# Optimization experiments

Hardware: AMD Instinct MI355X
Metric: run time of the kernel (lower is better)

The kernel has to match this reference:

```python
import jax, jax.numpy as jnp
import numpy as np

B = 8192          # batch (parallel RL envs)
LATENT = 32       # latent_size
CIN = 128         # original input_size (obs dim), c features
HID = 256         # hidden_size
ACT = 16          # num_actions
E = 8             # num_experts
GH = 128          # gate hidden size (hardcoded in module)
IN0 = LATENT + CIN    # layer-0 input dim (160)
INTER = HID + LATENT  # layer-1/2 input dim (288)
LN_EPS = 1e-5


def setup_inputs() -> dict:
    key = jax.random.key(0)
    ks = jax.random.split(key, 10)
    s = lambda k, shape, scale=1.0: jax.random.normal(k, shape, jnp.float32) * scale
    return {
        "z": s(ks[0], (B, LATENT)),
        "c": s(ks[1], (B, CIN)),
        # expert MLP params (kaiming-like small uniform scale stand-in)
        "w0": s(ks[2], (E, IN0, HID), 0.05),   "b0": jnp.full((E, HID), 0.01, jnp.float32),
        "w1": s(ks[3], (E, INTER, HID), 0.05), "b1": jnp.full((E, HID), 0.01, jnp.float32),
        "w2": s(ks[4], (E, INTER, ACT), 0.05), "b2": jnp.full((E, ACT), 0.01, jnp.float32),
        # gate MLP params
        "g0w": s(ks[5], (IN0, GH), 0.05), "g0b": jnp.zeros((GH,), jnp.float32),
        "g1w": s(ks[6], (GH, GH), 0.05),  "g1b": jnp.zeros((GH,), jnp.float32),
        "g2w": s(ks[7], (GH, E), 0.05),   "g2b": jnp.zeros((E,), jnp.float32),
        # LayerNorm on c
        "ln_g": jnp.ones((CIN,), jnp.float32),
        "ln_b": jnp.zeros((CIN,), jnp.float32),
    }


def _layer_norm(x, g, b):
    m = x.mean(-1, keepdims=True)
    v = ((x - m) ** 2).mean(-1, keepdims=True)
    return (x - m) / jnp.sqrt(v + LN_EPS) * g + b


def reference(z, c, w0, b0, w1, b1, w2, b2, g0w, g0b, g1w, g1b, g2w, g2b, ln_g, ln_b):
    cn = _layer_norm(c, ln_g, ln_b)                      # [B, CIN]
    x = jnp.concatenate([z, cn], axis=1)                 # [B, IN0]
    # gate: Linear-ELU-Linear-ELU-Linear, softmax over experts
    h = jax.nn.elu(x @ g0w + g0b)
    h = jax.nn.elu(h @ g1w + g1b)
    coeff = jax.nn.softmax(h @ g2w + g2b, axis=1)        # [B, E]

    layer_out = cn
    for w, b, act in ((w0, b0, True), (w1, b1, True), (w2, b2, False)):
        inp = jnp.concatenate([z, layer_out], axis=1)    # [B, in_dim]
        # per-expert GEMM then soft-mix (same math as coeff-mixed weight @ input)
        per = jnp.einsum('bi,eio->beo', inp, w)          # [B, E, out_dim]
        out = jnp.einsum('be,beo->bo', coeff, per) + coeff @ b  # [B, out_dim]
        layer_out = jax.nn.elu(out) if act else out
    return layer_out
```

## Files before the change

kernel.cpp:

```cpp
#include <hip/hip_runtime.h>
#include <math.h>

#define B_     8192
#define LATENT 32
#define CIN    128
#define HID    256
#define ACTD   16
#define NE     8
#define GH     128
#define IN0    160
#define INTER  288

typedef __attribute__((ext_vector_type(8))) _Float16 half8;
typedef __attribute__((ext_vector_type(4))) float    f32x4;
typedef __attribute__((ext_vector_type(4))) int      i32x4;

__device__ __forceinline__ float elu1(float x) { return x > 0.0f ? x : expm1f(x); }

__device__ __forceinline__ void gload16(const void* g, const char* lds) {
    __builtin_amdgcn_global_load_lds((const __attribute__((address_space(1))) void*)g,
                                     (__attribute__((address_space(3))) void*)lds, 16, 0, 0);
}
__device__ __forceinline__ half8 as_h8(i32x4 v) {
    union U { i32x4 a; half8 b; } u; u.a = v; return u.b;
}

__global__ __launch_bounds__(256) void k_prep_ln(
    const float* __restrict__ w0, const float* __restrict__ w1, const float* __restrict__ w2,
    const float* __restrict__ g0w, const float* __restrict__ g1w,
    const float* __restrict__ z, const float* __restrict__ c,
    const float* __restrict__ g, const float* __restrict__ bt,
    _Float16* __restrict__ T0, _Float16* __restrict__ T1, _Float16* __restrict__ T2,
    _Float16* __restrict__ G0, _Float16* __restrict__ G1,
    _Float16* __restrict__ X0, _Float16* __restrict__ X1, _Float16* __restrict__ X2)
{
    if (blockIdx.x < 484) {
        int gq = blockIdx.x * 256 + threadIdx.x;
        const float* src; int stride; size_t dst; _Float16* H;
        if (gq < 40960) {
            int e = gq / 5120, r = gq % 5120, o = r / 20, i0 = (r % 20) * 8;
            src = w0 + ((size_t)e * 160 + i0) * 256 + o; stride = 256;
            dst = ((size_t)e * 256 + o) * 160 + i0; H = T0;
        } else if (gq < 114688) {
            int t = gq - 40960;
            int e = t / 9216, r = t % 9216, o = r / 36, i0 = (r % 36) * 8;
            src = w1 + ((size_t)e * 288 + i0) * 256 + o; stride = 256;
            dst = ((size_t)e * 256 + o) * 288 + i0; H = T1;
        } else if (gq < 119296) {
            int t = gq - 114688;
            int e = t / 576, r = t % 576, o = r / 36, i0 = (r % 36) * 8;
            src = w2 + ((size_t)e * 288 + i0) * 16 + o; stride = 16;
            dst = ((size_t)e * 16 + o) * 288 + i0; H = T2;
        } else if (gq < 121856) {
            int t = gq - 119296;
            int o = t / 20, i0 = (t % 20) * 8;
            src = g0w + (size_t)i0 * 128 + o; stride = 128;
            dst = (size_t)o * 160 + i0; H = G0;
        } else if (gq < 123904) {
            int t = gq - 121856;
            int o = t / 16, i0 = (t % 16) * 8;
            src = g1w + (size_t)i0 * 128 + o; stride = 128;
            dst = (size_t)o * 128 + i0; H = G1;
        } else return;
        _Float16 hh[8];
        #pragma unroll
        for (int j = 0; j < 8; ++j) hh[j] = (_Float16)src[(size_t)j * stride];
        *(half8*)&H[dst] = *(const half8*)hh;
        return;
    }
    int gid = (blockIdx.x - 484) * 256 + threadIdx.x;
    int row = gid >> 6;
    int l = threadIdx.x & 63;
    const float* cr = c + (size_t)row * CIN;
    float v0 = cr[l], v1 = cr[l + 64];
    float s = v0 + v1;
    #pragma unroll
    for (int o = 32; o; o >>= 1) s += __shfl_xor(s, o);
    float mean = s * (1.0f / 128.0f);
    float d0 = v0 - mean, d1 = v1 - mean;
    float q = d0 * d0 + d1 * d1;
    #pragma unroll
    for (int o = 32; o; o >>= 1) q += __shfl_xor(q, o);
    float rstd = rsqrtf(q * (1.0f / 128.0f) + 1e-5f);
    float y0 = d0 * rstd * g[l] + bt[l];
    float y1 = d1 * rstd * g[l + 64] + bt[l + 64];
    size_t r0 = (size_t)row * IN0;
    X0[r0 + 32 + l] = (_Float16)y0;
    X0[r0 + 96 + l] = (_Float16)y1;
    if (l < LATENT) {
        _Float16 zv = (_Float16)z[(size_t)row * LATENT + l];
        X0[r0 + l] = zv;
        size_t r1 = (size_t)row * INTER;
        X1[r1 + l] = zv;
        X2[r1 + l] = zv;
    }
}

__global__ __launch_bounds__(128, 2) void k_gate_fused(
    const _Float16* __restrict__ X0, const _Float16* __restrict__ G0T,
    const _Float16* __restrict__ G1T,
    const float* __restrict__ g0b, const float* __restrict__ g1b,
    const float* __restrict__ g2w, const float* __restrict__ g2b,
    float* __restrict__ coeff)
{
    __shared__ __align__(16) char smem[86016];
    const int tid = threadIdx.x, wid = tid >> 6, l = tid & 63;
    const int brow = blockIdx.x * 32;
    const int rl16 = wid * 16;

    char* sG1  = smem + 40960;
    char* h1   = smem + 73728;
    float* wt_t = (float*)(smem + 81920);

    const int swz = (((l & 3) ^ ((l >> 3) & 3)) << 3);
    const int rq  = l >> 2;
    const int rdo = ((l & 15) << 6) + (((l >> 4) ^ ((l >> 1) & 3)) << 4);

    #pragma unroll
    for (int p = 0; p < 40; ++p) {
        if ((p & 1) != wid) continue;
        const int ks = p / 8, gg = p % 8;
        gload16(G0T + (size_t)(gg * 16 + rq) * IN0 + ks * 32 + swz, smem + p * 1024);
    }
    #pragma unroll
    for (int p = 0; p < 32; ++p) {
        if ((p & 1) != wid) continue;
        const int ks = p / 8, gg = p % 8;
        gload16(G1T + (size_t)(gg * 16 + rq) * GH + ks * 32 + swz, sG1 + p * 1024);
    }
    const _Float16* Ar0 = X0 + (size_t)(brow + rl16 + (l & 15)) * IN0 + (l >> 4) * 8;
    i32x4 a0[5];
    #pragma unroll
    for (int ks = 0; ks < 5; ++ks) a0[ks] = *(const i32x4*)(Ar0 + ks * 32);
    for (int idx = tid; idx < 1024; idx += 128)
        wt_t[(idx & 7) * 128 + (idx >> 3)] = g2w[(idx >> 3) * 8 + (idx & 7)];
    __syncthreads();

    f32x4 acc[8];
    #pragma unroll
    for (int nf = 0; nf < 8; ++nf) {
        float bv = g0b[nf * 16 + (l & 15)];
        acc[nf] = (f32x4){bv, bv, bv, bv};
    }
    #pragma unroll
    for (int ks = 0; ks < 5; ++ks)
        #pragma unroll
        for (int nf = 0; nf < 8; ++nf) {
            half8 b = *(const half8*)(smem + (size_t)(ks * 8 + nf) * 1024 + rdo);
            acc[nf] = __builtin_amdgcn_mfma_f32_16x16x32_f16(as_h8(a0[ks]), b, acc[nf], 0, 0, 0);
        }

    #pragma unroll
    for (int nf = 0; nf < 8; ++nf)
        #pragma unroll
        for (int r = 0; r < 4; ++r) {
            const int rloc = ((l >> 4) << 2) + r;
            const int row = rl16 + rloc;
            const int colb = (nf * 16 + (l & 15)) * 2;
            *(_Float16*)(h1 + row * 256 + (colb ^ ((rloc & 7) << 4))) = (_Float16)elu1(acc[nf][r]);
        }
    __syncthreads();

    i32x4 a1[4];
    #pragma unroll
    for (int ks = 0; ks < 4; ++ks) {
        const int row = rl16 + (l & 15);
        const int off = (ks * 64 + ((l >> 4) << 4)) ^ ((row & 7) << 4);
        a1[ks] = *(const i32x4*)(h1 + row * 256 + off);
    }

    #pragma unroll
    for (int nf = 0; nf < 8; ++nf) {
        float bv = g1b[nf * 16 + (l & 15)];
        acc[nf] = (f32x4){bv, bv, bv, bv};
    }
    #pragma unroll
    for (int ks = 0; ks < 4; ++ks)
        #pragma unroll
        for (int nf = 0; nf < 8; ++nf) {
            half8 b = *(const half8*)(sG1 + (size_t)(ks * 8 + nf) * 1024 + rdo);
            acc[nf] = __builtin_amdgcn_mfma_f32_16x16x32_f16(as_h8(a1[ks]), b, acc[nf], 0, 0, 0);
        }

    float pe[8][4];
    #pragma unroll
    for (int e = 0; e < 8; ++e)
        #pragma unroll
        for (int r = 0; r < 4; ++r) pe[e][r] = 0.f;
    #pragma unroll
    for (int nf = 0; nf < 8; ++nf) {
        float w_[8];
        #pragma unroll
        for (int e = 0; e < 8; ++e) w_[e] = wt_t[e * 128 + nf * 16 + (l & 15)];
        #pragma unroll
        for (int r = 0; r < 4; ++r) {
            float hv = elu1(acc[nf][r]);
            #pragma unroll
            for (int e = 0; e < 8; ++e) pe[e][r] = fmaf(hv, w_[e], pe[e][r]);
        }
    }
    #pragma unroll
    for (int off = 1; off < 16; off <<= 1)
        #pragma unroll
        for (int e = 0; e < 8; ++e)
            #pragma unroll
            for (int r = 0; r < 4; ++r) pe[e][r] += __shfl_xor(pe[e][r], off);

    if ((l & 15) == 0) {
        #pragma unroll
        for (int r = 0; r < 4; ++r) {
            float pv[8];
            float mx = -1e30f;
            #pragma unroll
            for (int e = 0; e < 8; ++e) { pv[e] = pe[e][r] + g2b[e]; mx = fmaxf(mx, pv[e]); }
            float s = 0.f;
            #pragma unroll
            for (int e = 0; e < 8; ++e) { pv[e] = expf(pv[e] - mx); s += pv[e]; }
            float inv = 1.0f / s;
            const int row = brow + rl16 + ((l >> 4) << 2) + r;
            #pragma unroll
            for (int e = 0; e < 8; ++e) coeff[(size_t)row * 8 + e] = pv[e] * inv;
        }
    }
}

template<int KS>
__global__ __launch_bounds__(256, 3) void k_moe_epar(
    const _Float16* __restrict__ A, const _Float16* __restrict__ Bw,
    const float* __restrict__ bias,
    const float* __restrict__ coeff,
    _Float16* __restrict__ outX)
{
    constexpr int K = KS * 32;
    __shared__ __align__(16) char smem[43008];

    const int tid = threadIdx.x, wid = tid >> 6, l = tid & 63;
    const int brow = (blockIdx.x & 127) * 64;
    const int bn   = (blockIdx.x >> 7) * 32;

    float* cfl = (float*)(smem + 40960);
    if (tid < 128) {
        f32x4 v = *(const f32x4*)&coeff[(size_t)(brow + (tid >> 1)) * 8 + (tid & 1) * 4];
        *(f32x4*)&cfl[tid * 4] = v;
    }

    const int swz = (((l & 3) ^ ((l >> 3) & 3)) << 3);
    const int rq  = l >> 2;
    const _Float16* sA = A + (size_t)(brow + wid * 16 + rq) * K + swz;
    const _Float16* sB2[2][2];
    #pragma unroll
    for (int e2 = 0; e2 < 2; ++e2)
        #pragma unroll
        for (int gg = 0; gg < 2; ++gg)
            sB2[e2][gg] = Bw + (size_t)((2 * wid + e2) * HID + bn + gg * 16 + rq) * K + swz;

    auto stage = [&](int bi, int k0) {
        char* buf = smem + bi * 20480;
        gload16(sA + k0, buf + wid * 1024);
        #pragma unroll
        for (int e2 = 0; e2 < 2; ++e2)
            #pragma unroll
            for (int gg = 0; gg < 2; ++gg)
                gload16(sB2[e2][gg] + k0,
                        buf + 4096 + (2 * wid + e2) * 2048 + gg * 1024);
    };

    const int rdo = ((l & 15) << 6) + (((l >> 4) ^ ((l >> 1) & 3)) << 4);
    f32x4 acc[2][4][2];
    #pragma unroll
    for (int e2 = 0; e2 < 2; ++e2)
        #pragma unroll
        for (int mf = 0; mf < 4; ++mf)
            #pragma unroll
            for (int nf = 0; nf < 2; ++nf) acc[e2][mf][nf] = (f32x4){0.f, 0.f, 0.f, 0.f};

    stage(0, 0);
    if (KS > 1) stage(1, 32);
    __syncthreads();

    for (int t = 0; t < KS; ++t) {
        const char* buf = smem + (t & 1) * 20480;
        half8 af[4], b0[2], b1[2];
        #pragma unroll
        for (int mf = 0; mf < 4; ++mf)
            af[mf] = *(const half8*)(buf + mf * 1024 + rdo);
        #pragma unroll
        for (int e2 = 0; e2 < 2; ++e2) {
            const char* be = buf + 4096 + (2 * wid + e2) * 2048;
            b0[e2] = *(const half8*)(be + rdo);
            b1[e2] = *(const half8*)(be + 1024 + rdo);
        }
        asm volatile("s_waitcnt lgkmcnt(0)" ::: "memory");
        __builtin_amdgcn_sched_barrier(0);
        __builtin_amdgcn_s_barrier();
        if (t + 2 < KS) stage(t & 1, (t + 2) * 32);
        __builtin_amdgcn_sched_barrier(0);

        __builtin_amdgcn_s_setprio(1);
        #pragma unroll
        for (int e2 = 0; e2 < 2; ++e2)
            #pragma unroll
            for (int mf = 0; mf < 4; ++mf) {
                acc[e2][mf][0] = __builtin_amdgcn_mfma_f32_16x16x32_f16(af[mf], b0[e2], acc[e2][mf][0], 0, 0, 0);
                acc[e2][mf][1] = __builtin_amdgcn_mfma_f32_16x16x32_f16(af[mf], b1[e2], acc[e2][mf][1], 0, 0, 0);
            }
        __builtin_amdgcn_s_setprio(0);

        if (t + 1 < KS) {
            if (t + 2 < KS) { asm volatile("s_waitcnt vmcnt(5)" ::: "memory"); }
            else            { asm volatile("s_waitcnt vmcnt(0)" ::: "memory"); }
            __builtin_amdgcn_s_barrier();
            __builtin_amdgcn_sched_barrier(0);
        }
    }

    const int e0 = 2 * wid, e1 = 2 * wid + 1;
    float bv0[2], bv1[2];
    #pragma unroll
    for (int nf = 0; nf < 2; ++nf) {
        bv0[nf] = bias[e0 * HID + bn + nf * 16 + (l & 15)];
        bv1[nf] = bias[e1 * HID + bn + nf * 16 + (l & 15)];
    }
    __syncthreads();
    float* red = (float*)smem;
    #pragma unroll
    for (int mf = 0; mf < 4; ++mf) {
        const int rb = mf * 16 + ((l >> 4) << 2);
        #pragma unroll
        for (int r = 0; r < 4; ++r) {
            float c0 = cfl[(rb + r) * 8 + e0];
            float c1 = cfl[(rb + r) * 8 + e1];
            #pragma unroll
            for (int nf = 0; nf < 2; ++nf) {
                float s = (acc[0][mf][nf][r] + bv0[nf]) * c0
                        + (acc[1][mf][nf][r] + bv1[nf]) * c1;
                red[wid * 2304 + (rb + r) * 36 + nf * 16 + (l & 15)] = s;
            }
        }
    }
    __syncthreads();

    const int row = tid >> 2, c0_ = (tid & 3) * 8;
    f32x4 s0 = {0.f, 0.f, 0.f, 0.f}, s1 = {0.f, 0.f, 0.f, 0.f};
    #pragma unroll
    for (int w = 0; w < 4; ++w) {
        s0 += *(const f32x4*)&red[w * 2304 + row * 36 + c0_];
        s1 += *(const f32x4*)&red[w * 2304 + row * 36 + c0_ + 4];
    }
    _Float16 hh[8];
    #pragma unroll
    for (int j = 0; j < 4; ++j) {
        hh[j]     = (_Float16)elu1(s0[j]);
        hh[4 + j] = (_Float16)elu1(s1[j]);
    }
    size_t o = (size_t)(brow + row) * INTER + 32 + bn + c0_;
    *(half8*)&outX[o] = *(const half8*)hh;
}

__global__ __launch_bounds__(128, 2) void k_final(
    const _Float16* __restrict__ X2, const _Float16* __restrict__ T2,
    const float* __restrict__ b2, const float* __restrict__ cf,
    float* __restrict__ out)
{
    __shared__ __align__(16) char smem[73728];
    const int tid = threadIdx.x, wid = tid >> 6, l = tid & 63;
    const int brow = blockIdx.x * 32;

    const _Float16* Ar = X2 + (size_t)(brow + wid * 16 + (l & 15)) * INTER + (l >> 4) * 8;
    i32x4 a_[9];
    #pragma unroll
    for (int ks = 0; ks < 9; ++ks) a_[ks] = *(const i32x4*)(Ar + ks * 32);

    const int swz = (((l & 3) ^ ((l >> 3) & 3)) << 3);
    const int rq  = l >> 2;
    #pragma unroll
    for (int p = 0; p < 72; ++p) {
        if ((p & 1) != wid) continue;
        const int ks = p / 8, gg = p % 8;
        gload16(T2 + (size_t)(gg * 16 + rq) * INTER + ks * 32 + swz, smem + p * 1024);
    }

    const int rdo = ((l & 15) << 6) + (((l >> 4) ^ ((l >> 1) & 3)) << 4);
    f32x4 acc[8];
    #pragma unroll
    for (int nf = 0; nf < 8; ++nf) {
        float bv = b2[nf * 16 + (l & 15)];
        acc[nf] = (f32x4){bv, bv, bv, bv};
    }
    #pragma unroll
    for (int ks = 0; ks < 9; ++ks) {
        switch (ks) {
            case 0: asm volatile("s_waitcnt vmcnt(32)" ::: "memory"); break;
            case 1: asm volatile("s_waitcnt vmcnt(28)" ::: "memory"); break;
            case 2: asm volatile("s_waitcnt vmcnt(24)" ::: "memory"); break;
            case 3: asm volatile("s_waitcnt vmcnt(20)" ::: "memory"); break;
            case 4: asm volatile("s_waitcnt vmcnt(16)" ::: "memory"); break;
            case 5: asm volatile("s_waitcnt vmcnt(12)" ::: "memory"); break;
            case 6: asm volatile("s_waitcnt vmcnt(8)"  ::: "memory"); break;
            case 7: asm volatile("s_waitcnt vmcnt(4)"  ::: "memory"); break;
            default: asm volatile("s_waitcnt vmcnt(0)" ::: "memory"); break;
        }
        __builtin_amdgcn_s_barrier();
        __builtin_amdgcn_sched_barrier(0);
        if (ks == 0) {
            #pragma unroll
            for (int k2 = 0; k2 < 9; ++k2) asm volatile("" : "+v"(a_[k2]));
        }
        #pragma unroll
        for (int nf = 0; nf < 8; ++nf) {
            half8 b = *(const half8*)(smem + (size_t)(ks * 8 + nf) * 1024 + rdo);
            acc[nf] = __builtin_amdgcn_mfma_f32_16x16x32_f16(as_h8(a_[ks]), b, acc[nf], 0, 0, 0);
        }
    }

    #pragma unroll
    for (int r = 0; r < 4; ++r) {
        const int row = brow + wid * 16 + ((l >> 4) << 2) + r;
        const float* cr = cf + (size_t)row * 8;
        float s = 0.f;
        #pragma unroll
        for (int e = 0; e < 8; ++e) s = fmaf(cr[e], acc[e][r], s);
        out[(size_t)row * ACTD + (l & 15)] = s;
    }
}

extern "C" void kernel_launch(void* const* d_in, const int* in_sizes, int n_in,
                              void* d_out, int out_size, void* d_ws, size_t ws_size,
                              hipStream_t stream)
{
    (void)in_sizes; (void)n_in; (void)out_size; (void)ws_size;
    const float* z   = (const float*)d_in[0];
    const float* c   = (const float*)d_in[1];
    const float* w0  = (const float*)d_in[2];
    const float* b0  = (const float*)d_in[3];
    const float* w1  = (const float*)d_in[4];
    const float* b1  = (const float*)d_in[5];
    const float* w2  = (const float*)d_in[6];
    const float* b2  = (const float*)d_in[7];
    const float* g0w = (const float*)d_in[8];
    const float* g0b = (const float*)d_in[9];
    const float* g1w = (const float*)d_in[10];
    const float* g1b = (const float*)d_in[11];
    const float* g2w = (const float*)d_in[12];
    const float* g2b = (const float*)d_in[13];
    const float* lng = (const float*)d_in[14];
    const float* lnb = (const float*)d_in[15];
    float* out = (float*)d_out;

    char* p = (char*)d_ws;
    auto alloc = [&](size_t n) { char* r = p; p += (n + 255) & ~(size_t)255; return r; };
    _Float16* X0  = (_Float16*)alloc((size_t)B_ * IN0 * 2);
    _Float16* X1  = (_Float16*)alloc((size_t)B_ * INTER * 2);
    _Float16* X2  = (_Float16*)alloc((size_t)B_ * INTER * 2);
    float* cf  = (float*)alloc((size_t)B_ * NE * 4);
    _Float16* T0  = (_Float16*)alloc((size_t)NE * IN0 * HID * 2);
    _Float16* T1  = (_Float16*)alloc((size_t)NE * INTER * HID * 2);
    _Float16* T2  = (_Float16*)alloc((size_t)NE * INTER * ACTD * 2);
    _Float16* G0T = (_Float16*)alloc((size_t)IN0 * GH * 2);
    _Float16* G1T = (_Float16*)alloc((size_t)GH * GH * 2);

    k_prep_ln<<<dim3(484 + B_ / 4), dim3(256), 0, stream>>>(
        w0, w1, w2, g0w, g1w, z, c, lng, lnb,
        T0, T1, T2, G0T, G1T, X0, X1, X2);

    k_gate_fused<<<dim3(256), dim3(128), 0, stream>>>(
        X0, G0T, G1T, g0b, g1b, g2w, g2b, cf);

    k_moe_epar<5><<<dim3(1024), dim3(256), 0, stream>>>(X0, T0, b0, cf, X1);
    k_moe_epar<9><<<dim3(1024), dim3(256), 0, stream>>>(X1, T1, b1, cf, X2);

    k_final<<<dim3(256), dim3(128), 0, stream>>>(X2, T2, b2, cf, out);
}
```

Baseline: 65.29 us.

## Replace double-buffered BK32 MoE pipeline with single-buffer BK64 stages

After: 68.58 us. 5.1% more time.

```diff
diff --git a/kernel.cpp b/kernel.cpp
--- a/kernel.cpp
+++ b/kernel.cpp
@@ -225,13 +225,14 @@
 }
 
 template<int KS>
-__global__ __launch_bounds__(256, 3) void k_moe_epar(
+__global__ __launch_bounds__(256, 3) void k_moe_bk64(
     const _Float16* __restrict__ A, const _Float16* __restrict__ Bw,
     const float* __restrict__ bias,
     const float* __restrict__ coeff,
     _Float16* __restrict__ outX)
 {
-    constexpr int K = KS * 32;
+    constexpr int K  = KS * 32;
+    constexpr int NP = (KS + 1) / 2;
     __shared__ __align__(16) char smem[43008];
 
     const int tid = threadIdx.x, wid = tid >> 6, l = tid & 63;
@@ -254,15 +255,19 @@
         for (int gg = 0; gg < 2; ++gg)
             sB2[e2][gg] = Bw + (size_t)((2 * wid + e2) * HID + bn + gg * 16 + rq) * K + swz;
 
-    auto stage = [&](int bi, int k0) {
-        char* buf = smem + bi * 20480;
-        gload16(sA + k0, buf + wid * 1024);
-        #pragma unroll
-        for (int e2 = 0; e2 < 2; ++e2)
-            #pragma unroll
-            for (int gg = 0; gg < 2; ++gg)
-                gload16(sB2[e2][gg] + k0,
-                        buf + 4096 + (2 * wid + e2) * 2048 + gg * 1024);
+    auto stage = [&](int p) {
+        const int ks0 = 2 * p;
+        #pragma unroll
+        for (int h = 0; h < 2; ++h) {
+            if (ks0 + h >= KS) break;
+            gload16(sA + (ks0 + h) * 32, smem + h * 4096 + wid * 1024);
+            #pragma unroll
+            for (int e2 = 0; e2 < 2; ++e2)
+                #pragma unroll
+                for (int gg = 0; gg < 2; ++gg)
+                    gload16(sB2[e2][gg] + (ks0 + h) * 32,
+                            smem + 8192 + h * 16384 + (2 * wid + e2) * 2048 + gg * 1024);
+        }
     };
 
     const int rdo = ((l & 15) << 6) + (((l >> 4) ^ ((l >> 1) & 3)) << 4);
@@ -274,44 +279,42 @@
             #pragma unroll
             for (int nf = 0; nf < 2; ++nf) acc[e2][mf][nf] = (f32x4){0.f, 0.f, 0.f, 0.f};
 
-    stage(0, 0);
-    if (KS > 1) stage(1, 32);
+    stage(0);
     __syncthreads();
 
-    for (int t = 0; t < KS; ++t) {
-        const char* buf = smem + (t & 1) * 20480;
-        half8 af[4], b0[2], b1[2];
-        #pragma unroll
-        for (int mf = 0; mf < 4; ++mf)
-            af[mf] = *(const half8*)(buf + mf * 1024 + rdo);
-        #pragma unroll
-        for (int e2 = 0; e2 < 2; ++e2) {
-            const char* be = buf + 4096 + (2 * wid + e2) * 2048;
-            b0[e2] = *(const half8*)(be + rdo);
-            b1[e2] = *(const half8*)(be + 1024 + rdo);
+    for (int p = 0; p < NP; ++p) {
+        if (p > 0) {
+            asm volatile("s_waitcnt vmcnt(0)" ::: "memory");
+            __builtin_amdgcn_s_barrier();
+            __builtin_amdgcn_sched_barrier(0);
+        }
+        #pragma unroll
+        for (int h = 0; h < 2; ++h) {
+            if (2 * p + h >= KS) break;
+            half8 af[4], b0[2], b1[2];
+            #pragma unroll
+            for (int mf = 0; mf < 4; ++mf)
+                af[mf] = *(const half8*)(smem + h * 4096 + mf * 1024 + rdo);
+            #pragma unroll
+            for (int e2 = 0; e2 < 2; ++e2) {
+                const char* be = smem + 8192 + h * 16384 + (2 * wid + e2) * 2048;
+                b0[e2] = *(const half8*)(be + rdo);
+                b1[e2] = *(const half8*)(be + 1024 + rdo);
+            }
+            __builtin_amdgcn_s_setprio(1);
+            #pragma unroll
+            for (int e2 = 0; e2 < 2; ++e2)
+                #pragma unroll
+                for (int mf = 0; mf < 4; ++mf) {
+                    acc[e2][mf][0] = __builtin_amdgcn_mfma_f32_16x16x32_f16(af[mf], b0[e2], acc[e2][mf][0], 0, 0, 0);
+                    acc[e2][mf][1] = __builtin_amdgcn_mfma_f32_16x16x32_f16(af[mf], b1[e2], acc[e2][mf][1], 0, 0, 0);
+                }
+            __builtin_amdgcn_s_setprio(0);
         }
         asm volatile("s_waitcnt lgkmcnt(0)" ::: "memory");
         __builtin_amdgcn_sched_barrier(0);
         __builtin_amdgcn_s_barrier();
-        if (t + 2 < KS) stage(t & 1, (t + 2) * 32);
-        __builtin_amdgcn_sched_barrier(0);
-
-        __builtin_amdgcn_s_setprio(1);
-        #pragma unroll
-        for (int e2 = 0; e2 < 2; ++e2)
-            #pragma unroll
-            for (int mf = 0; mf < 4; ++mf) {
-                acc[e2][mf][0] = __builtin_amdgcn_mfma_f32_16x16x32_f16(af[mf], b0[e2], acc[e2][mf][0], 0, 0, 0);
-                acc[e2][mf][1] = __builtin_amdgcn_mfma_f32_16x16x32_f16(af[mf], b1[e2], acc[e2][mf][1], 0, 0, 0);
-            }
-        __builtin_amdgcn_s_setprio(0);
-
-        if (t + 1 < KS) {
-            if (t + 2 < KS) { asm volatile("s_waitcnt vmcnt(5)" ::: "memory"); }
-            else            { asm volatile("s_waitcnt vmcnt(0)" ::: "memory"); }
-            __builtin_amdgcn_s_barrier();
-            __builtin_amdgcn_sched_barrier(0);
-        }
+        if (p + 1 < NP) stage(p + 1);
     }
 
     const int e0 = 2 * wid, e1 = 2 * wid + 1;
@@ -321,7 +324,6 @@
         bv0[nf] = bias[e0 * HID + bn + nf * 16 + (l & 15)];
         bv1[nf] = bias[e1 * HID + bn + nf * 16 + (l & 15)];
     }
-    __syncthreads();
     float* red = (float*)smem;
     #pragma unroll
     for (int mf = 0; mf < 4; ++mf) {
@@ -466,8 +468,8 @@
     k_gate_fused<<<dim3(256), dim3(128), 0, stream>>>(
         X0, G0T, G1T, g0b, g1b, g2w, g2b, cf);
 
-    k_moe_epar<5><<<dim3(1024), dim3(256), 0, stream>>>(X0, T0, b0, cf, X1);
-    k_moe_epar<9><<<dim3(1024), dim3(256), 0, stream>>>(X1, T1, b1, cf, X2);
+    k_moe_bk64<5><<<dim3(1024), dim3(256), 0, stream>>>(X0, T0, b0, cf, X1);
+    k_moe_bk64<9><<<dim3(1024), dim3(256), 0, stream>>>(X1, T1, b1, cf, X2);
 
     k_final<<<dim3(256), dim3(128), 0, stream>>>(X2, T2, b2, cf, out);
 }
```
